# Optimization experiments

Hardware: AMD Instinct MI355X
Metric: run time of the kernel (lower is better)

## Reference

```python
import jax, jax.numpy as jnp
import numpy as np

B, L, D, A = 64, 196, 2048, 1024  # batch, locations, hidden_size, att_hid_size


def setup_inputs() -> dict:
    key = jax.random.key(0)
    ks = jax.random.split(key, 8)
    scale = 0.02
    return {
        "att_features": jax.random.normal(ks[0], (B, L, D), dtype=jnp.float32),
        "h": jax.random.normal(ks[1], (B, D), dtype=jnp.float32),
        "W_att": jax.random.normal(ks[2], (D, A), dtype=jnp.float32) * scale,
        "b_att": jnp.zeros((A,), dtype=jnp.float32),
        "W_h": jax.random.normal(ks[3], (D, A), dtype=jnp.float32) * scale,
        "b_h": jnp.zeros((A,), dtype=jnp.float32),
        "w_alpha": jax.random.normal(ks[4], (A, 1), dtype=jnp.float32) * scale,
        "b_alpha": jnp.zeros((1,), dtype=jnp.float32),
    }


def reference(att_features, h, W_att, b_att, W_h, b_h, w_alpha, b_alpha):
    b = att_features.shape[0]
    d = att_features.shape[-1]
    locations = att_features.size // b // d
    af = att_features.reshape(b, locations, d)            # [B, L, D]
    p_att = af @ W_att + b_att                            # [B, L, A]
    p_h = (h @ W_h + b_h)[:, None, :]                     # [B, 1, A]
    scores = (jnp.tanh(p_att + p_h) @ w_alpha + b_alpha)[..., 0]  # [B, L]
    weights = jax.nn.softmax(scores, axis=1)              # [B, L]
    weighted = jnp.einsum('bl,bld->bd', weights, af)      # [B, D]
    return weighted, weights
```

## Files before the change

kernel.cpp:

```cpp
#include <hip/hip_runtime.h>


typedef unsigned short u16;
typedef u16 u16x8 __attribute__((ext_vector_type(8)));
typedef __bf16 bf16x8 __attribute__((ext_vector_type(8)));
typedef float f32x4 __attribute__((ext_vector_type(4)));

#define B_ 64
#define L_ 196
#define D_ 2048
#define A_ 1024
#define M_ (B_ * L_)

__device__ __forceinline__ u16 f2bf(float x) {
  unsigned u = __float_as_uint(x);
  unsigned r = (u + 0x7fffu + ((u >> 16) & 1u)) >> 16;
  return (u16)r;
}

__device__ __forceinline__ float tanh_fast(float x) {
  float e = __expf(2.0f * x);
  return 1.0f - 2.0f / (e + 1.0f);
}

__device__ __forceinline__ void gload_lds16(const void* g, void* l) {
  __builtin_amdgcn_global_load_lds(
      (const __attribute__((address_space(1))) void*)g,
      (__attribute__((address_space(3))) void*)l, 16, 0, 0);
}

__global__ __launch_bounds__(256) void prep_k(
    const float* __restrict__ af, u16* __restrict__ afb,
    const float* __restrict__ W, u16* __restrict__ WT,
    const float* __restrict__ h, const float* __restrict__ Wh,
    float* __restrict__ ph) {
  __shared__ float smem[2112];
  const int bid = blockIdx.x;
  const int t = threadIdx.x;
  if (bid < 256) {
    const int ag = bid & 3, bg = (bid >> 2) & 7, dc = bid >> 5;
    const int d0 = dc * 256;
    for (int i = t; i < 2048; i += 256)
      smem[i] = h[(size_t)(bg * 8 + (i >> 8)) * D_ + d0 + (i & 255)];
    __syncthreads();
    const int a = ag * 256 + t;
    float acc[8] = {};
#pragma unroll 8
    for (int d = 0; d < 256; ++d) {
      float wv = Wh[(size_t)(d0 + d) * A_ + a];
#pragma unroll
      for (int bb = 0; bb < 8; ++bb) acc[bb] += smem[bb * 256 + d] * wv;
    }
#pragma unroll
    for (int bb = 0; bb < 8; ++bb)
      atomicAdd(&ph[(size_t)(bg * 8 + bb) * A_ + a], acc[bb]);
  } else if (bid < 2304) {
    const int tb = bid - 256;
    const int n0 = (tb & 31) * 32, k0 = (tb >> 5) * 32;
    const int tx = t & 31, ty = t >> 5;
    float (*tt)[33] = (float (*)[33])smem;
#pragma unroll
    for (int i = 0; i < 4; ++i)
      tt[ty + i * 8][tx] = W[(size_t)(k0 + ty + i * 8) * A_ + n0 + tx];
    __syncthreads();
#pragma unroll
    for (int i = 0; i < 4; ++i)
      WT[(size_t)(n0 + ty + i * 8) * D_ + k0 + tx] = f2bf(tt[tx][ty + i * 8]);
  } else {
    const int cb = bid - 2304;
    const size_t n = (size_t)M_ * D_;
    for (size_t e = ((size_t)cb * 256 + t) * 8; e < n;
         e += (size_t)2048 * 256 * 8) {
      float4 v0 = *(const float4*)(af + e);
      float4 v1 = *(const float4*)(af + e + 4);
      u16x8 p;
      p[0] = f2bf(v0.x); p[1] = f2bf(v0.y); p[2] = f2bf(v0.z); p[3] = f2bf(v0.w);
      p[4] = f2bf(v1.x); p[5] = f2bf(v1.y); p[6] = f2bf(v1.z); p[7] = f2bf(v1.w);
      *(u16x8*)(afb + e) = p;
    }
  }
}

__global__ __launch_bounds__(512, 2) void gemm8_k(
    const u16* __restrict__ afb, const u16* __restrict__ WT,
    const float* __restrict__ ph, const float* __restrict__ batt,
    const float* __restrict__ bh, const float* __restrict__ walpha,
    float* __restrict__ scores4) {
  __shared__ __align__(16) u16 As[2][2][8192];
  __shared__ __align__(16) u16 Bs[2][2][8192];
  const int tid = threadIdx.x;
  const int lane = tid & 63;
  const int wid = tid >> 6;
  const int wr = wid >> 2;
  const int wc = wid & 3;
  const int wchalf = wc >> 1, wcl = wc & 1;
  const int fr = lane & 15, fq = lane >> 4;

  const int xcd = blockIdx.x & 7, idx = blockIdx.x >> 3;
  const int wg = (xcd < 4 ? xcd * 25 : 100 + (xcd - 4) * 24) + idx;
  const int m0 = (wg >> 2) * 256;
  const int n0 = (wg & 3) * 256;

  int rowc[2], colc[2];
#pragma unroll
  for (int r = 0; r < 2; ++r) {
    int c = r * 512 + tid;
    int s = c >> 6, cw = c & 63;
    rowc[r] = (s >> 1) * 16 + (cw >> 2);
    colc[r] = (s & 1) * 32 + ((((cw & 3) * 16) ^ (((cw >> 5) & 1) * 32)) >> 1);
  }
  const u16* srcA[2][2];
  const u16* srcB[2][2];
#pragma unroll
  for (int hh = 0; hh < 2; ++hh)
#pragma unroll
    for (int r = 0; r < 2; ++r) {
      srcA[hh][r] = afb + (size_t)(m0 + hh * 128 + rowc[r]) * D_ + colc[r];
      srcB[hh][r] = WT + (size_t)(n0 + hh * 128 + rowc[r]) * D_ + colc[r];
    }

  const int laneA = (lane & 15) * 64 + (((lane >> 4) * 16) ^ ((lane & 8) << 2));

  f32x4 acc[8][4] = {};
  u16x8 areg[4][2], breg[4][2];

#define STG_A(BUF, H, KT)                                                    \
  do {                                                                       \
    gload_lds16(srcA[H][0] + (size_t)(KT) * 64, &As[BUF][H][wid * 512]);     \
    gload_lds16(srcA[H][1] + (size_t)(KT) * 64, &As[BUF][H][4096 + wid * 512]); \
  } while (0)
#define STG_B(BUF, H, KT)                                                    \
  do {                                                                       \
    gload_lds16(srcB[H][0] + (size_t)(KT) * 64, &Bs[BUF][H][wid * 512]);     \
    gload_lds16(srcB[H][1] + (size_t)(KT) * 64, &Bs[BUF][H][4096 + wid * 512]); \
  } while (0)
#define LDA_HALF(BF, MH)                                                     \
  do {                                                                       \
    _Pragma("unroll") for (int q = 0; q < 4; ++q) {                          \
      areg[q][0] = *(const u16x8*)&As[BF][wr][((((MH)*4 + q) * 2 + 0) * 1024 + laneA) >> 1]; \
      areg[q][1] = *(const u16x8*)&As[BF][wr][((((MH)*4 + q) * 2 + 1) * 1024 + laneA) >> 1]; \
    }                                                                        \
  } while (0)
#define LDB_PAIR(BF, NQ)                                                     \
  do {                                                                       \
    _Pragma("unroll") for (int nn = 0; nn < 2; ++nn) {                       \
      breg[(NQ)*2 + nn][0] = *(const u16x8*)&Bs[BF][wchalf][(((wcl * 4 + (NQ)*2 + nn) * 2 + 0) * 1024 + laneA) >> 1]; \
      breg[(NQ)*2 + nn][1] = *(const u16x8*)&Bs[BF][wchalf][(((wcl * 4 + (NQ)*2 + nn) * 2 + 1) * 1024 + laneA) >> 1]; \
    }                                                                        \
  } while (0)
#define MM_QUAD(MH, NQ)                                                      \
  do {                                                                       \
    _Pragma("unroll") for (int q = 0; q < 4; ++q)                            \
    _Pragma("unroll") for (int nn = 0; nn < 2; ++nn)                         \
    _Pragma("unroll") for (int kh = 0; kh < 2; ++kh)                         \
      acc[(MH)*4 + q][(NQ)*2 + nn] = __builtin_amdgcn_mfma_f32_16x16x32_bf16( \
          __builtin_bit_cast(bf16x8, areg[q][kh]),                           \
          __builtin_bit_cast(bf16x8, breg[(NQ)*2 + nn][kh]),                 \
          acc[(MH)*4 + q][(NQ)*2 + nn], 0, 0, 0);                            \
  } while (0)
#define PH_PRE()                                                             \
  do {                                                                       \
    __builtin_amdgcn_s_barrier();                                            \
    __builtin_amdgcn_s_setprio(1);                                           \
  } while (0)
#define PH_POST()                                                            \
  do {                                                                       \
    __builtin_amdgcn_s_setprio(0);                                           \
    __builtin_amdgcn_s_barrier();                                            \
  } while (0)
#define KTILE(BF, T, MODE)                                                   \
  do {                                                                       \
    LDA_HALF(BF, 0); LDB_PAIR(BF, 0); LDB_PAIR(BF, 1);                       \
    if ((MODE) <= 1) STG_A((BF) ^ 1, 1, (T) + 1);                            \
    PH_PRE(); MM_QUAD(0, 0); MM_QUAD(0, 1); PH_POST();                       \
    LDA_HALF(BF, 1);                                                         \
    if ((MODE) == 0) { STG_B(BF, 0, (T) + 2); STG_B(BF, 1, (T) + 2);         \
                       STG_A(BF, 0, (T) + 2); }                              \
    PH_PRE(); MM_QUAD(1, 0); MM_QUAD(1, 1);                                  \
    __builtin_amdgcn_s_setprio(0);                                           \
    if ((MODE) == 0) asm volatile("s_waitcnt vmcnt(6)" ::: "memory");        \
    if ((MODE) == 1) asm volatile("s_waitcnt vmcnt(0)" ::: "memory");        \
    if ((MODE) <= 1) __builtin_amdgcn_s_barrier();                           \
  } while (0)

  STG_B(0, 0, 0); STG_B(0, 1, 0); STG_A(0, 0, 0); STG_A(0, 1, 0);
  STG_B(1, 0, 1); STG_B(1, 1, 1); STG_A(1, 0, 1);
  asm volatile("s_waitcnt vmcnt(6)" ::: "memory");
  __builtin_amdgcn_s_barrier();

#pragma unroll 1
  for (int it = 0; it < 15; ++it) {
    const int t = it * 2;
    KTILE(0, t, 0);
    KTILE(1, t + 1, 0);
  }
  KTILE(0, 30, 1);
  KTILE(1, 31, 2);

  const int gnb = n0 + wc * 64 + fr;
  float wa[4], bsv[4], p0[4], p1[4], p2[4];
  const int b0 = m0 / L_;
  const int s1 = (b0 + 1) * L_, s2 = (b0 + 2) * L_;
  const int b1 = (b0 + 1 > 63) ? 63 : b0 + 1;
  const int b2 = (b0 + 2 > 63) ? 63 : b0 + 2;
#pragma unroll
  for (int ni = 0; ni < 4; ++ni) {
    const int gn = gnb + ni * 16;
    wa[ni] = walpha[gn];
    bsv[ni] = batt[gn] + bh[gn];
    p0[ni] = ph[(size_t)b0 * A_ + gn];
    p1[ni] = ph[(size_t)b1 * A_ + gn];
    p2[ni] = ph[(size_t)b2 * A_ + gn];
  }
  __syncthreads();
  float (*redp)[128][4] = (float (*)[128][4])As;
#pragma unroll
  for (int mi = 0; mi < 8; ++mi) {
#pragma unroll
    for (int rr = 0; rr < 4; ++rr) {
      const int lr = mi * 16 + fq * 4 + rr;
      const int gm = m0 + wr * 128 + lr;
      float sp = 0.f;
#pragma unroll
      for (int ni = 0; ni < 4; ++ni) {
        const float pv = (gm >= s2) ? p2[ni] : ((gm >= s1) ? p1[ni] : p0[ni]);
        const float p = acc[mi][ni][rr] + pv + bsv[ni];
        sp += tanh_fast(p) * wa[ni];
      }
      sp += __shfl_xor(sp, 1);
      sp += __shfl_xor(sp, 2);
      sp += __shfl_xor(sp, 4);
      sp += __shfl_xor(sp, 8);
      if (fr == 0) redp[wr][lr][wc] = sp;
    }
  }
  __syncthreads();
  if (tid < 256) {
    f32x4 v = ((const f32x4*)redp)[tid];
    scores4[(size_t)(n0 >> 8) * M_ + m0 + tid] = v[0] + v[1] + v[2] + v[3];
  }
}

__global__ __launch_bounds__(256) void wsum_sm_k(const u16* __restrict__ afb,
                                                 const float* __restrict__ s4,
                                                 float* __restrict__ out) {
  __shared__ float wl[256];
  __shared__ float part[256][8];
  __shared__ float red[4];
  const int b = blockIdx.y;
  const int t = threadIdx.x;

  float s = -1e30f;
  if (t < L_) {
    const int i = b * L_ + t;
    s = s4[i] + s4[M_ + i] + s4[2 * M_ + i] + s4[3 * M_ + i];
  }
  float m = s;
#pragma unroll
  for (int o = 32; o; o >>= 1) m = fmaxf(m, __shfl_xor(m, o));
  if ((t & 63) == 0) red[t >> 6] = m;
  __syncthreads();
  m = fmaxf(fmaxf(red[0], red[1]), fmaxf(red[2], red[3]));
  float e = (t < L_) ? __expf(s - m) : 0.f;
  float sum = e;
#pragma unroll
  for (int o = 32; o; o >>= 1) sum += __shfl_xor(sum, o);
  __syncthreads();
  if ((t & 63) == 0) red[t >> 6] = sum;
  __syncthreads();
  sum = red[0] + red[1] + red[2] + red[3];
  const float w = e / sum;
  wl[t] = w;
  if (t < L_ && blockIdx.x == 0) out[(size_t)B_ * D_ + b * L_ + t] = w;
  __syncthreads();

  const int lq = t >> 6;
  const int dl = t & 63;
  const int d8 = blockIdx.x * 64 + dl;
  float acc[8] = {};
  for (int l = lq * 49; l < lq * 49 + 49; ++l) {
    u16x8 v = *(const u16x8*)(afb + (size_t)(b * L_ + l) * D_ + d8 * 8);
    float ww = wl[l];
#pragma unroll
    for (int j = 0; j < 8; ++j)
      acc[j] += ww * __uint_as_float((unsigned)v[j] << 16);
  }
#pragma unroll
  for (int j = 0; j < 8; ++j) part[t][j] = acc[j];
  __syncthreads();
  if (t < 64) {
    float4 o0, o1;
    o0.x = part[dl][0] + part[64 + dl][0] + part[128 + dl][0] + part[192 + dl][0];
    o0.y = part[dl][1] + part[64 + dl][1] + part[128 + dl][1] + part[192 + dl][1];
    o0.z = part[dl][2] + part[64 + dl][2] + part[128 + dl][2] + part[192 + dl][2];
    o0.w = part[dl][3] + part[64 + dl][3] + part[128 + dl][3] + part[192 + dl][3];
    o1.x = part[dl][4] + part[64 + dl][4] + part[128 + dl][4] + part[192 + dl][4];
    o1.y = part[dl][5] + part[64 + dl][5] + part[128 + dl][5] + part[192 + dl][5];
    o1.z = part[dl][6] + part[64 + dl][6] + part[128 + dl][6] + part[192 + dl][6];
    o1.w = part[dl][7] + part[64 + dl][7] + part[128 + dl][7] + part[192 + dl][7];
    *(float4*)(out + (size_t)b * D_ + d8 * 8) = o0;
    *(float4*)(out + (size_t)b * D_ + d8 * 8 + 4) = o1;
  }
}

extern "C" void kernel_launch(void* const* d_in, const int* in_sizes, int n_in,
                              void* d_out, int out_size, void* d_ws, size_t ws_size,
                              hipStream_t stream) {
  const float* af    = (const float*)d_in[0];
  const float* h     = (const float*)d_in[1];
  const float* W_att = (const float*)d_in[2];
  const float* b_att = (const float*)d_in[3];
  const float* W_h   = (const float*)d_in[4];
  const float* b_h   = (const float*)d_in[5];
  const float* w_al  = (const float*)d_in[6];
  float* out = (float*)d_out;
  char* ws = (char*)d_ws;

  u16* afb       = (u16*)ws;
  u16* WT        = (u16*)(ws + 0x3200000);
  float* ph      = (float*)(ws + 0x3600000);
  float* scores4 = (float*)(ws + 0x3640000);

  hipMemsetAsync(ph, 0, 256u << 10, stream);
  prep_k<<<4352, 256, 0, stream>>>(af, afb, W_att, WT, h, W_h, ph);
  gemm8_k<<<196, 512, 0, stream>>>(afb, WT, ph, b_att, b_h, w_al, scores4);
  wsum_sm_k<<<dim3(4, 64), 256, 0, stream>>>(afb, scores4, out);
}
```

Measured before the change: 118.7 us.

## Shrink GEMM M-tile to 224 rows to launch 224 blocks

Changes the GEMM tile from 256x256 to 224x256, so M=12544 splits into 56 row tiles and the grid becomes 224 blocks instead of 196. This aims to fill all 256 compute units better and cut wave-quantization idle time. The A staging is reworked so that a partial fourth load covers only half the lanes, the accumulators drop to 7 fragments per wave, and the wait counts are adjusted. In exchange, arithmetic intensity per block is lower and the A loads are less regular.

```diff
diff --git a/kernel.cpp b/kernel.cpp
--- a/kernel.cpp
+++ b/kernel.cpp
@@ -86,7 +86,7 @@
     const float* __restrict__ ph, const float* __restrict__ batt,
     const float* __restrict__ bh, const float* __restrict__ walpha,
     float* __restrict__ scores4) {
-  __shared__ __align__(16) u16 As[2][2][8192];
+  __shared__ __align__(16) u16 As[2][2][7168];
   __shared__ __align__(16) u16 Bs[2][2][8192];
   const int tid = threadIdx.x;
   const int lane = tid & 63;
@@ -96,10 +96,25 @@
   const int wchalf = wc >> 1, wcl = wc & 1;
   const int fr = lane & 15, fq = lane >> 4;
 
-  const int xcd = blockIdx.x & 7, idx = blockIdx.x >> 3;
-  const int wg = (xcd < 4 ? xcd * 25 : 100 + (xcd - 4) * 24) + idx;
-  const int m0 = (wg >> 2) * 256;
+  const int wg = (blockIdx.x & 7) * 28 + (blockIdx.x >> 3);
+  const int m0 = (wg >> 2) * 224;
   const int n0 = (wg & 3) * 256;
+
+  const u16* srcA4[4];
+  int hfA[4], dstA[4];
+#pragma unroll
+  for (int r = 0; r < 4; ++r) {
+    const int c = (r < 3) ? (r * 512 + tid) : (1536 + wid * 32 + (lane & 31));
+    const int hf = c >= 896;
+    const int cl = c - hf * 896;
+    const int s = cl >> 6, cw = cl & 63;
+    const int row = (s >> 1) * 16 + (cw >> 2);
+    const int col = (s & 1) * 32 + ((((cw & 3) * 16) ^ (((cw >> 5) & 1) * 32)) >> 1);
+    srcA4[r] = afb + (size_t)(m0 + hf * 112 + row) * D_ + col;
+    const int cb = (r < 3) ? (r * 512 + wid * 64) : (1536 + wid * 32);
+    hfA[r] = cb >= 896;
+    dstA[r] = (cb - hfA[r] * 896) * 8;
+  }
 
   int rowc[2], colc[2];
 #pragma unroll
@@ -109,36 +124,36 @@
     rowc[r] = (s >> 1) * 16 + (cw >> 2);
     colc[r] = (s & 1) * 32 + ((((cw & 3) * 16) ^ (((cw >> 5) & 1) * 32)) >> 1);
   }
-  const u16* srcA[2][2];
   const u16* srcB[2][2];
 #pragma unroll
   for (int hh = 0; hh < 2; ++hh)
 #pragma unroll
-    for (int r = 0; r < 2; ++r) {
-      srcA[hh][r] = afb + (size_t)(m0 + hh * 128 + rowc[r]) * D_ + colc[r];
+    for (int r = 0; r < 2; ++r)
       srcB[hh][r] = WT + (size_t)(n0 + hh * 128 + rowc[r]) * D_ + colc[r];
-    }
 
   const int laneA = (lane & 15) * 64 + (((lane >> 4) * 16) ^ ((lane & 8) << 2));
 
-  f32x4 acc[8][4] = {};
+  f32x4 acc[7][4] = {};
   u16x8 areg[4][2], breg[4][2];
 
-#define STG_A(BUF, H, KT)                                                    \
-  do {                                                                       \
-    gload_lds16(srcA[H][0] + (size_t)(KT) * 64, &As[BUF][H][wid * 512]);     \
-    gload_lds16(srcA[H][1] + (size_t)(KT) * 64, &As[BUF][H][4096 + wid * 512]); \
+#define STG_A4(BUF, KT)                                                      \
+  do {                                                                       \
+    gload_lds16(srcA4[0] + (size_t)(KT) * 64, &As[BUF][hfA[0]][dstA[0]]);    \
+    gload_lds16(srcA4[1] + (size_t)(KT) * 64, &As[BUF][hfA[1]][dstA[1]]);    \
+    gload_lds16(srcA4[2] + (size_t)(KT) * 64, &As[BUF][hfA[2]][dstA[2]]);    \
+    if (lane < 32)                                                           \
+      gload_lds16(srcA4[3] + (size_t)(KT) * 64, &As[BUF][hfA[3]][dstA[3]]);  \
   } while (0)
 #define STG_B(BUF, H, KT)                                                    \
   do {                                                                       \
     gload_lds16(srcB[H][0] + (size_t)(KT) * 64, &Bs[BUF][H][wid * 512]);     \
     gload_lds16(srcB[H][1] + (size_t)(KT) * 64, &Bs[BUF][H][4096 + wid * 512]); \
   } while (0)
-#define LDA_HALF(BF, MH)                                                     \
-  do {                                                                       \
-    _Pragma("unroll") for (int q = 0; q < 4; ++q) {                          \
-      areg[q][0] = *(const u16x8*)&As[BF][wr][((((MH)*4 + q) * 2 + 0) * 1024 + laneA) >> 1]; \
-      areg[q][1] = *(const u16x8*)&As[BF][wr][((((MH)*4 + q) * 2 + 1) * 1024 + laneA) >> 1]; \
+#define LDA_P(BF, FBASE, NF)                                                 \
+  do {                                                                       \
+    _Pragma("unroll") for (int q = 0; q < (NF); ++q) {                       \
+      areg[q][0] = *(const u16x8*)&As[BF][wr][((((FBASE) + q) * 2 + 0) * 1024 + laneA) >> 1]; \
+      areg[q][1] = *(const u16x8*)&As[BF][wr][((((FBASE) + q) * 2 + 1) * 1024 + laneA) >> 1]; \
     }                                                                        \
   } while (0)
 #define LDB_PAIR(BF, NQ)                                                     \
@@ -148,15 +163,15 @@
       breg[(NQ)*2 + nn][1] = *(const u16x8*)&Bs[BF][wchalf][(((wcl * 4 + (NQ)*2 + nn) * 2 + 1) * 1024 + laneA) >> 1]; \
     }                                                                        \
   } while (0)
-#define MM_QUAD(MH, NQ)                                                      \
-  do {                                                                       \
-    _Pragma("unroll") for (int q = 0; q < 4; ++q)                            \
-    _Pragma("unroll") for (int nn = 0; nn < 2; ++nn)                         \
+#define MM_P(FBASE, NF)                                                      \
+  do {                                                                       \
+    _Pragma("unroll") for (int q = 0; q < (NF); ++q)                         \
+    _Pragma("unroll") for (int nn = 0; nn < 4; ++nn)                         \
     _Pragma("unroll") for (int kh = 0; kh < 2; ++kh)                         \
-      acc[(MH)*4 + q][(NQ)*2 + nn] = __builtin_amdgcn_mfma_f32_16x16x32_bf16( \
+      acc[(FBASE) + q][nn] = __builtin_amdgcn_mfma_f32_16x16x32_bf16(        \
           __builtin_bit_cast(bf16x8, areg[q][kh]),                           \
-          __builtin_bit_cast(bf16x8, breg[(NQ)*2 + nn][kh]),                 \
-          acc[(MH)*4 + q][(NQ)*2 + nn], 0, 0, 0);                            \
+          __builtin_bit_cast(bf16x8, breg[nn][kh]), acc[(FBASE) + q][nn],    \
+          0, 0, 0);                                                          \
   } while (0)
 #define PH_PRE()                                                             \
   do {                                                                       \
@@ -170,29 +185,28 @@
   } while (0)
 #define KTILE(BF, T, MODE)                                                   \
   do {                                                                       \
-    LDA_HALF(BF, 0); LDB_PAIR(BF, 0); LDB_PAIR(BF, 1);                       \
-    if ((MODE) <= 1) STG_A((BF) ^ 1, 1, (T) + 1);                            \
-    PH_PRE(); MM_QUAD(0, 0); MM_QUAD(0, 1); PH_POST();                       \
-    LDA_HALF(BF, 1);                                                         \
-    if ((MODE) == 0) { STG_B(BF, 0, (T) + 2); STG_B(BF, 1, (T) + 2);         \
-                       STG_A(BF, 0, (T) + 2); }                              \
-    PH_PRE(); MM_QUAD(1, 0); MM_QUAD(1, 1);                                  \
+    LDA_P(BF, 0, 4); LDB_PAIR(BF, 0); LDB_PAIR(BF, 1);                       \
+    if ((MODE) <= 1) STG_A4((BF) ^ 1, (T) + 1);                              \
+    PH_PRE(); MM_P(0, 4); PH_POST();                                         \
+    LDA_P(BF, 4, 3);                                                         \
+    if ((MODE) == 0) { STG_B(BF, 0, (T) + 2); STG_B(BF, 1, (T) + 2); }       \
+    PH_PRE(); MM_P(4, 3);                                                    \
     __builtin_amdgcn_s_setprio(0);                                           \
-    if ((MODE) == 0) asm volatile("s_waitcnt vmcnt(6)" ::: "memory");        \
+    if ((MODE) == 0) asm volatile("s_waitcnt vmcnt(2)" ::: "memory");        \
     if ((MODE) == 1) asm volatile("s_waitcnt vmcnt(0)" ::: "memory");        \
     if ((MODE) <= 1) __builtin_amdgcn_s_barrier();                           \
   } while (0)
 
-  STG_B(0, 0, 0); STG_B(0, 1, 0); STG_A(0, 0, 0); STG_A(0, 1, 0);
-  STG_B(1, 0, 1); STG_B(1, 1, 1); STG_A(1, 0, 1);
-  asm volatile("s_waitcnt vmcnt(6)" ::: "memory");
+  STG_A4(0, 0);
+  STG_B(0, 0, 0); STG_B(0, 1, 0);
+  STG_B(1, 0, 1); STG_B(1, 1, 1);
+  asm volatile("s_waitcnt vmcnt(2)" ::: "memory");
   __builtin_amdgcn_s_barrier();
 
 #pragma unroll 1
   for (int it = 0; it < 15; ++it) {
-    const int t = it * 2;
-    KTILE(0, t, 0);
-    KTILE(1, t + 1, 0);
+    KTILE(0, 2 * it, 0);
+    KTILE(1, 2 * it + 1, 0);
   }
   KTILE(0, 30, 1);
   KTILE(1, 31, 2);
@@ -213,13 +227,13 @@
     p2[ni] = ph[(size_t)b2 * A_ + gn];
   }
   __syncthreads();
-  float (*redp)[128][4] = (float (*)[128][4])As;
-#pragma unroll
-  for (int mi = 0; mi < 8; ++mi) {
+  float (*redp)[112][4] = (float (*)[112][4])As;
+#pragma unroll
+  for (int mi = 0; mi < 7; ++mi) {
 #pragma unroll
     for (int rr = 0; rr < 4; ++rr) {
       const int lr = mi * 16 + fq * 4 + rr;
-      const int gm = m0 + wr * 128 + lr;
+      const int gm = m0 + wr * 112 + lr;
       float sp = 0.f;
 #pragma unroll
       for (int ni = 0; ni < 4; ++ni) {
@@ -235,7 +249,7 @@
     }
   }
   __syncthreads();
-  if (tid < 256) {
+  if (tid < 224) {
     f32x4 v = ((const f32x4*)redp)[tid];
     scores4[(size_t)(n0 >> 8) * M_ + m0 + tid] = v[0] + v[1] + v[2] + v[3];
   }
@@ -323,6 +337,6 @@
 
   hipMemsetAsync(ph, 0, 256u << 10, stream);
   prep_k<<<4352, 256, 0, stream>>>(af, afb, W_att, WT, h, W_h, ph);
-  gemm8_k<<<196, 512, 0, stream>>>(afb, WT, ph, b_att, b_h, w_al, scores4);
+  gemm8_k<<<224, 512, 0, stream>>>(afb, WT, ph, b_att, b_h, w_al, scores4);
   wsum_sm_k<<<dim3(4, 64), 256, 0, stream>>>(afb, scores4, out);
 }
```

Measured after the change: 121.7 us. +2.6%, slower.
